# Optimization experiments

Measured on AMD Instinct MI355X. Metric: run time of the kernel, lower is better.

## Reference

```python
import jax, jax.numpy as jnp
import numpy as np

H = 8          # multihead_num (also groups of the Conv1d)
LN_EPS = 1e-5  # torch.nn.LayerNorm default


def _gconv(x, w):
    """Grouped Conv1d, kernel=3, stride=1, 'same' reflect padding, no bias.
    x: [B, C_in, L], w: [C_out, C_in//H, K] (torch OIH layout)."""
    xp = jnp.pad(x, ((0, 0), (0, 0), (1, 1)), mode='reflect')
    return jax.lax.conv_general_dilated(
        xp, w, window_strides=(1,), padding='VALID',
        feature_group_count=H, dimension_numbers=('NCH', 'OIH', 'NCH'))


def setup_inputs() -> dict:
    key = jax.random.key(0)
    ks = jax.random.split(key, 5)
    B, C, L = 8, 512, 1024
    q = jax.random.normal(ks[0], (B, C, L), jnp.float32)
    k = jax.random.normal(ks[1], (B, C, L), jnp.float32)
    # causal mask: 1 above the diagonal -> -1e9 subtracted pre-softmax
    mask = jnp.triu(jnp.ones((L, L), jnp.float32), k=1)
    # init_params: std = sqrt(2 / (C_out + C_in/groups))
    std = float(np.sqrt(2.0 / (C + C // H)))
    wq = jax.random.normal(ks[2], (C, C // H, 3), jnp.float32) * std
    wk = jax.random.normal(ks[3], (C, C // H, 3), jnp.float32) * std
    wv = jax.random.normal(ks[4], (C, C // H, 3), jnp.float32) * std
    gamma = jnp.ones((C,), jnp.float32)
    beta = jnp.zeros((C,), jnp.float32)
    return {"q": q, "k": k, "mask": mask, "wq": wq, "wk": wk, "wv": wv,
            "gamma": gamma, "beta": beta}


def reference(q, k, mask, wq, wk, wv, gamma, beta):
    init = q                               # residual branch, [B, C, L]
    B, C, L = q.shape
    D = C // H                             # head dim
    v = k                                  # inputs list of length 2 -> v = k

    qh = _gconv(q, wq).reshape(B, H, D, L)  # split(dim=1)+cat(dim=0) == head axis
    kh = _gconv(k, wk).reshape(B, H, D, L)
    vh = _gconv(v, wv).reshape(B, H, D, L)

    # scores: q^T k per head; NOTE: scaled by sqrt(multihead_num), as in source
    scores = jnp.einsum('bhdl,bhdm->bhlm', qh, kh) / jnp.sqrt(
        jnp.asarray(H, qh.dtype))
    scores = scores - 1e9 * mask           # mask broadcast over [B, H]
    att = jax.nn.softmax(scores, axis=-1)  # dropout p=0.0 -> identity

    # o = att @ v^T, then concat heads along channel (head-major order)
    o = jnp.einsum('bhlm,bhdm->blhd', att, vh).reshape(B, L, C)

    # residual add + LayerNorm over channel dim
    x = o + jnp.swapaxes(init, 1, 2)       # [B, L, C]
    mu = jnp.mean(x, axis=-1, keepdims=True)
    var = jnp.mean(jnp.square(x - mu), axis=-1, keepdims=True)
    y = (x - mu) * jax.lax.rsqrt(var + LN_EPS) * gamma + beta
    return jnp.swapaxes(y, 1, 2)           # [B, C, L]
```

## Files before the change

kernel.cpp:

```cpp
#include <hip/hip_runtime.h>
#include <math.h>

#define H 8
#define B 8
#define C 512
#define L 1024
#define D 64
#define LDK 72

typedef __attribute__((ext_vector_type(4))) float f32x4;
typedef __attribute__((ext_vector_type(8))) short bf16x8;

static __device__ __forceinline__ short f2bf(float x) {
    union { float f; unsigned u; } v; v.f = x;
    unsigned r = v.u + 0x7FFFu + ((v.u >> 16) & 1u);
    return (short)(r >> 16);
}
static __device__ __forceinline__ short f2bf_fast(float x) {
    union { float f; unsigned u; } v; v.f = x;
    return (short)((v.u + 0x8000u) >> 16);
}
static __device__ __forceinline__ int pack2(short a, short b) {
    return (int)((unsigned short)a | ((unsigned)(unsigned short)b << 16));
}
static __device__ __forceinline__ float bfs2f(short v) {
    union { unsigned u; float f; } w; w.u = ((unsigned)(unsigned short)v) << 16;
    return w.f;
}
static __device__ __forceinline__ void async16(const void* g, void* s) {
    __builtin_amdgcn_global_load_lds(
        (const __attribute__((address_space(1))) int*)g,
        (__attribute__((address_space(3))) int*)s, 16, 0, 0);
}

__global__ __launch_bounds__(256) void wprep_kernel(
    const float* __restrict__ wq, const float* __restrict__ wk,
    const float* __restrict__ wv, short* __restrict__ wtg)
{
    int idx = blockIdx.x * 256 + threadIdx.x;
    int jj    = idx & 7;
    int quad  = (idx >> 3) & 3;
    int d     = (idx >> 5) & 63;
    int r     = idx >> 11;
    int khalf = r & 1;  r >>= 1;
    int t     = r % 3;  r /= 3;
    int h     = r & 7;
    int conv  = r >> 3;
    const float* w = (conv == 0) ? wq : (conv == 1) ? wk : wv;
    int j_in = khalf * 32 + quad * 8 + jj;
    float v = w[(h * 64 + d) * 192 + j_in * 3 + t];
    if (conv == 0) v *= 0.51012254f;
    wtg[idx] = f2bf(v);
}

__global__ __launch_bounds__(256) void conv_kv_kernel(
    const float* __restrict__ k, const short* __restrict__ wtg,
    short* __restrict__ kh, short* __restrict__ vh)
{
    int bx   = blockIdx.x;
    int xcd  = bx & 7;
    int g    = bx >> 3;
    int bh   = xcd + 8 * (g & 7);
    int tile = g >> 3;
    int h    = bh & 7;
    int b    = bh >> 3;

    __shared__ __align__(16) short xT[66 * LDK];

    int l0  = tile * 64;
    int tid = threadIdx.x;
    int wave = tid >> 6, lane = tid & 63;
    int n = lane & 15, quad = lane >> 4;

    const float* xb = k + (size_t)(b * C + h * 64) * L + l0;

    const short* wb0 = wtg + (size_t)((1 * 8 + h) * 6) * 2048;
    const short* wb1 = wtg + (size_t)((2 * 8 + h) * 6) * 2048;
    bf16x8 wf[3][2], wf2[3][2];
    #pragma unroll
    for (int t = 0; t < 3; t++)
        #pragma unroll
        for (int kk = 0; kk < 2; kk++) {
            wf[t][kk]  = *(const bf16x8*)(wb0 + (t * 2 + kk) * 2048
                                          + (wave * 16 + n) * 32 + quad * 8);
            wf2[t][kk] = *(const bf16x8*)(wb1 + (t * 2 + kk) * 2048
                                          + (wave * 16 + n) * 32 + quad * 8);
        }

    {
        #pragma unroll
        for (int s = 0; s < 4; s++) {
            int idx = tid + s * 256;
            int j = idx >> 4, seg = idx & 15;
            float4 v = *(const float4*)(xb + j * L + seg * 4);
            int p = 1 + seg * 4;
            xT[(p + 0) * LDK + j] = f2bf(v.x);
            xT[(p + 1) * LDK + j] = f2bf(v.y);
            xT[(p + 2) * LDK + j] = f2bf(v.z);
            xT[(p + 3) * LDK + j] = f2bf(v.w);
        }
        if (tid < 64) {
            int gl = (l0 == 0) ? 1 : (l0 - 1);
            xT[0 * LDK + tid] = f2bf(k[(size_t)(b * C + h * 64 + tid) * L + gl]);
        } else if (tid < 128) {
            int j2 = tid - 64;
            int gl = (l0 + 64 >= L) ? (L - 2) : (l0 + 64);
            xT[65 * LDK + j2] = f2bf(k[(size_t)(b * C + h * 64 + j2) * L + gl]);
        }
    }
    __syncthreads();

    f32x4 acc[4], acc2[4];
    #pragma unroll
    for (int bl = 0; bl < 4; bl++) {
        acc[bl]  = (f32x4){0.f, 0.f, 0.f, 0.f};
        acc2[bl] = (f32x4){0.f, 0.f, 0.f, 0.f};
    }

    #pragma unroll
    for (int bl = 0; bl < 4; bl++)
        #pragma unroll
        for (int t = 0; t < 3; t++)
            #pragma unroll
            for (int kk = 0; kk < 2; kk++) {
                bf16x8 bf = *(const bf16x8*)&xT[(bl * 16 + n + t) * LDK
                                                + kk * 32 + quad * 8];
                acc[bl]  = __builtin_amdgcn_mfma_f32_16x16x32_bf16(
                    wf[t][kk],  bf, acc[bl],  0, 0, 0);
                acc2[bl] = __builtin_amdgcn_mfma_f32_16x16x32_bf16(
                    wf2[t][kk], bf, acc2[bl], 0, 0, 0);
            }

    {
        short* ob = kh + ((size_t)(bh * 16 + tile)) * 4096;
        int ch = wave * 2 + (quad >> 1);
        #pragma unroll
        for (int bl = 0; bl < 4; bl++) {
            int l = bl * 16 + n;
            int phys = ch ^ (l & 7);
            int2 v;
            v.x = pack2(f2bf(acc[bl][0]), f2bf(acc[bl][1]));
            v.y = pack2(f2bf(acc[bl][2]), f2bf(acc[bl][3]));
            *(int2*)&ob[l * 64 + phys * 8 + (quad & 1) * 4] = v;
        }
    }
    __syncthreads();
    #pragma unroll
    for (int bl = 0; bl < 4; bl++)
        #pragma unroll
        for (int r = 0; r < 4; r++) {
            int d = wave * 16 + quad * 4 + r;
            int l = bl * 16 + n;
            int phys = (bl * 2 + (n >> 3)) ^ (d & 7);
            xT[d * 64 + phys * 8 + (n & 7)] = f2bf(acc2[bl][r]);
        }
    __syncthreads();
    short* vb = vh + ((size_t)(bh * 16 + tile)) * 4096;
    #pragma unroll
    for (int jj = 0; jj < 2; jj++) {
        int i = tid + jj * 256;
        *(int4*)(vb + i * 8) = *(const int4*)&xT[i * 8];
    }
}

__global__ __launch_bounds__(256, 4) void flash_kernel(
    const float* __restrict__ q, const short* __restrict__ wtg,
    const short* __restrict__ kh, const short* __restrict__ vh,
    short* __restrict__ ot)
{
    __shared__ __align__(16) short lds[20480];
    short* xT = &lds[4096];

    int bx  = blockIdx.x;
    int xcd = bx & 7;
    int g   = bx >> 3;
    int bh  = xcd + 8 * (g & 7);
    int qt  = 15 - (g >> 3);
    int h  = bh & 7, b = bh >> 3;

    int tid  = threadIdx.x;
    int wave = tid >> 6, lane = tid & 63;
    int n    = lane & 15, quad = lane >> 4;
    int l0   = qt * 64;

    {
        const float* xb = q + (size_t)(b * C + h * 64) * L + l0;
        const short* wb0 = wtg + (size_t)((0 * 8 + h) * 6) * 2048;
        bf16x8 wf[3][2];
        #pragma unroll
        for (int t = 0; t < 3; t++)
            #pragma unroll
            for (int kk = 0; kk < 2; kk++)
                wf[t][kk] = *(const bf16x8*)(wb0 + (t * 2 + kk) * 2048
                                             + (wave * 16 + n) * 32 + quad * 8);
        #pragma unroll
        for (int s = 0; s < 4; s++) {
            int idx = tid + s * 256;
            int j = idx >> 4, seg = idx & 15;
            float4 v = *(const float4*)(xb + j * L + seg * 4);
            int p = 1 + seg * 4;
            xT[(p + 0) * LDK + j] = f2bf(v.x);
            xT[(p + 1) * LDK + j] = f2bf(v.y);
            xT[(p + 2) * LDK + j] = f2bf(v.z);
            xT[(p + 3) * LDK + j] = f2bf(v.w);
        }
        if (tid < 64) {
            int gl = (l0 == 0) ? 1 : (l0 - 1);
            xT[0 * LDK + tid] = f2bf(q[(size_t)(b * C + h * 64 + tid) * L + gl]);
        } else if (tid < 128) {
            int j2 = tid - 64;
            int gl = (l0 + 64 >= L) ? (L - 2) : (l0 + 64);
            xT[65 * LDK + j2] = f2bf(q[(size_t)(b * C + h * 64 + j2) * L + gl]);
        }
        __syncthreads();

        f32x4 acc[4];
        #pragma unroll
        for (int bl = 0; bl < 4; bl++) acc[bl] = (f32x4){0.f, 0.f, 0.f, 0.f};
        #pragma unroll
        for (int bl = 0; bl < 4; bl++)
            #pragma unroll
            for (int t = 0; t < 3; t++)
                #pragma unroll
                for (int kk = 0; kk < 2; kk++) {
                    bf16x8 bf = *(const bf16x8*)&xT[(bl * 16 + n + t) * LDK
                                                    + kk * 32 + quad * 8];
                    acc[bl] = __builtin_amdgcn_mfma_f32_16x16x32_bf16(
                        wf[t][kk], bf, acc[bl], 0, 0, 0);
                }
        __syncthreads();
        int ch = wave * 2 + (quad >> 1);
        #pragma unroll
        for (int bl = 0; bl < 4; bl++) {
            int l = bl * 16 + n;
            int phys = ch ^ (l & 7);
            int2 v;
            v.x = pack2(f2bf(acc[bl][0]), f2bf(acc[bl][1]));
            v.y = pack2(f2bf(acc[bl][2]), f2bf(acc[bl][3]));
            *(int2*)&lds[l * 64 + phys * 8 + (quad & 1) * 4] = v;
        }
    }

    const short* Kbase = kh + (size_t)bh * 65536;
    const short* Vbase = vh + (size_t)bh * 65536;

    {
        int ci = wave * 64 + lane;
        async16((const int4*)Kbase + ci,        lds + 4096 + wave * 512);
        async16((const int4*)Kbase + ci + 256,  lds + 4096 + 2048 + wave * 512);
        async16((const int4*)Vbase + ci,        lds + 8192 + wave * 512);
        async16((const int4*)Vbase + ci + 256,  lds + 8192 + 2048 + wave * 512);
    }
    __syncthreads();

    int ph0 = quad ^ (n & 7);
    int ph1 = (quad + 4) ^ (n & 7);

    bf16x8 qa0 = *(const bf16x8*)&lds[(wave * 16 + n) * 64 + ph0 * 8];
    bf16x8 qa1 = *(const bf16x8*)&lds[(wave * 16 + n) * 64 + ph1 * 8];

    const bf16x8 ones = {16256,16256,16256,16256,16256,16256,16256,16256};

    f32x4 O0 = {0.f,0.f,0.f,0.f}, O1 = O0, O2 = O0, O3 = O0;
    f32x4 Lacc = {0.f,0.f,0.f,0.f};

    int prow   = wave * 16 + n;
    int pswz   = n & 7;

    for (int kt = 0; kt <= qt; kt++) {
        if (kt > 0) __syncthreads();
        if (kt < qt) {
            const short* Kg = Kbase + (size_t)(kt + 1) * 4096;
            const short* Vg = Vbase + (size_t)(kt + 1) * 4096;
            int koff = 4096 + (((kt + 1) & 1)) * 8192;
            int ci = wave * 64 + lane;
            async16((const int4*)Kg + ci,       lds + koff + wave * 512);
            async16((const int4*)Kg + ci + 256, lds + koff + 2048 + wave * 512);
            async16((const int4*)Vg + ci,       lds + koff + 4096 + wave * 512);
            async16((const int4*)Vg + ci + 256, lds + koff + 4096 + 2048 + wave * 512);
        }
        const short* Kb = lds + 4096 + (kt & 1) * 8192;
        const short* Vb = Kb + 4096;

        f32x4 s[4];
        #pragma unroll
        for (int bk = 0; bk < 4; bk++) {
            int row = bk * 16 + n;
            bf16x8 kb0 = *(const bf16x8*)&Kb[row * 64 + ph0 * 8];
            bf16x8 kb1 = *(const bf16x8*)&Kb[row * 64 + ph1 * 8];
            f32x4 acc = {0.f,0.f,0.f,0.f};
            acc = __builtin_amdgcn_mfma_f32_16x16x32_bf16(kb0, qa0, acc, 0, 0, 0);
            acc = __builtin_amdgcn_mfma_f32_16x16x32_bf16(kb1, qa1, acc, 0, 0, 0);
            s[bk] = acc;
        }

        if (kt == qt) {
            #pragma unroll
            for (int bk = 0; bk < 4; bk++)
                #pragma unroll
                for (int r = 0; r < 4; r++)
                    if (bk * 16 + quad * 4 + r > wave * 16 + n)
                        s[bk][r] = -INFINITY;
        }

        #pragma unroll
        for (int bk = 0; bk < 4; bk++) {
            int pch = (bk * 2 + (quad >> 1)) ^ pswz;
            int2 v;
            v.x = pack2(f2bf_fast(__builtin_amdgcn_exp2f(s[bk][0] - 20.f)),
                        f2bf_fast(__builtin_amdgcn_exp2f(s[bk][1] - 20.f)));
            v.y = pack2(f2bf_fast(__builtin_amdgcn_exp2f(s[bk][2] - 20.f)),
                        f2bf_fast(__builtin_amdgcn_exp2f(s[bk][3] - 20.f)));
            *(int2*)&lds[prow * 64 + pch * 8 + (quad & 1) * 4] = v;
        }

        bf16x8 pa0 = *(const bf16x8*)&lds[prow * 64 + ph0 * 8];
        bf16x8 pa1 = *(const bf16x8*)&lds[prow * 64 + ph1 * 8];

        Lacc = __builtin_amdgcn_mfma_f32_16x16x32_bf16(pa0, ones, Lacc, 0, 0, 0);
        Lacc = __builtin_amdgcn_mfma_f32_16x16x32_bf16(pa1, ones, Lacc, 0, 0, 0);

        #pragma unroll
        for (int bk = 0; bk < 4; bk++) {
            int row = bk * 16 + n;
            bf16x8 v0 = *(const bf16x8*)&Vb[row * 64 + ph0 * 8];
            bf16x8 v1 = *(const bf16x8*)&Vb[row * 64 + ph1 * 8];
            f32x4* Op = (bk == 0) ? &O0 : (bk == 1) ? &O1 : (bk == 2) ? &O2 : &O3;
            *Op = __builtin_amdgcn_mfma_f32_16x16x32_bf16(pa0, v0, *Op, 0, 0, 0);
            *Op = __builtin_amdgcn_mfma_f32_16x16x32_bf16(pa1, v1, *Op, 0, 0, 0);
        }
    }

    float inv[4];
    #pragma unroll
    for (int r = 0; r < 4; r++) inv[r] = 1.f / Lacc[r];

    __syncthreads();
    short* Eb = lds + 4096;
    #pragma unroll
    for (int bk = 0; bk < 4; bk++) {
        f32x4* Op = (bk == 0) ? &O0 : (bk == 1) ? &O1 : (bk == 2) ? &O2 : &O3;
        #pragma unroll
        for (int r = 0; r < 4; r++)
            Eb[(bk * 16 + n) * LDK + wave * 16 + quad * 4 + r] =
                f2bf_fast((*Op)[r] * inv[r]);
    }
    __syncthreads();
    #pragma unroll
    for (int jj = 0; jj < 2; jj++) {
        int i = tid + jj * 256;
        int d = i >> 3, seg = i & 7;
        int4 v = *(const int4*)&Eb[d * LDK + seg * 8];
        *(int4*)(ot + ((size_t)(b * C) + h * 64 + d) * L + qt * 64 + seg * 8) = v;
    }
}

__global__ __launch_bounds__(512) void ln_kernel(
    const short* __restrict__ ot, const float* __restrict__ q,
    const float* __restrict__ gamma, const float* __restrict__ beta,
    float* __restrict__ y)
{
    int bx = blockIdx.x;
    int tile = bx & 31;
    int b = bx >> 5;
    int l0 = tile * 32;
    int tid = threadIdx.x;
    int li_ = tid & 31, cs = tid >> 5;

    __shared__ float sp[16][33], ssp[16][33];
    __shared__ float mu_s[32], rs_s[32];

    size_t base = ((size_t)b * C + cs * 32) * L + l0 + li_;
    const short* otp = ot + base;
    const float* qp  = q + base;

    float xr[32];
    float s = 0.f, ss = 0.f;
    #pragma unroll
    for (int cc = 0; cc < 32; cc++) {
        float x = bfs2f(otp[(size_t)cc * L]) + qp[(size_t)cc * L];
        xr[cc] = x;
        s += x; ss += x * x;
    }
    sp[cs][li_] = s; ssp[cs][li_] = ss;
    __syncthreads();
    if (tid < 32) {
        float t1 = 0.f, t2 = 0.f;
        #pragma unroll
        for (int j = 0; j < 16; j++) { t1 += sp[j][tid]; t2 += ssp[j][tid]; }
        float mean = t1 * (1.f / 512.f);
        float var  = t2 * (1.f / 512.f) - mean * mean;
        mu_s[tid] = mean;
        rs_s[tid] = rsqrtf(var + 1e-5f);
    }
    __syncthreads();
    float mu = mu_s[li_], rs = rs_s[li_];
    float* yp = y + base;
    #pragma unroll
    for (int cc = 0; cc < 32; cc++) {
        int c = cs * 32 + cc;
        yp[(size_t)cc * L] = (xr[cc] - mu) * rs * gamma[c] + beta[c];
    }
}

extern "C" void kernel_launch(void* const* d_in, const int* in_sizes, int n_in,
                              void* d_out, int out_size, void* d_ws, size_t ws_size,
                              hipStream_t stream)
{
    const float* q     = (const float*)d_in[0];
    const float* k     = (const float*)d_in[1];
    const float* wq    = (const float*)d_in[3];
    const float* wk    = (const float*)d_in[4];
    const float* wv    = (const float*)d_in[5];
    const float* gamma = (const float*)d_in[6];
    const float* beta  = (const float*)d_in[7];
    float* y = (float*)d_out;

    const size_t N = (size_t)B * H * L * D;
    short* kh  = (short*)d_ws;
    short* vh  = kh + N;
    short* ot  = vh + N;
    short* wtg = ot + N;

    wprep_kernel<<<1152, 256, 0, stream>>>(wq, wk, wv, wtg);
    conv_kv_kernel<<<B * H * (L / 64), 256, 0, stream>>>(k, wtg, kh, vh);
    flash_kernel<<<B * H * (L / 64), 256, 0, stream>>>(q, wtg, kh, vh, ot);
    ln_kernel<<<B * (L / 32), 512, 0, stream>>>(ot, q, gamma, beta, y);
}
```

Before: 127.9 us.

## Fuse weight prep into conv kernels and residual add into flash epilogue

Removes the separate weight-preparation kernel: each conv and flash block now loads its fp32 weight rows directly and converts them to bf16 fragments in registers. The flash epilogue stages the output in fp32 LDS, adds the residual q there, and writes the sum as bf16, so the LayerNorm kernel no longer reads q. This saves a launch and one fp32 read pass of q in the LN kernel. In exchange, weights are converted redundantly in every block, and the residual is now rounded to bf16 before LayerNorm, which lowers precision.

Result: slower. 135.3 us (+5.8%).

```diff
diff --git a/kernel.cpp b/kernel.cpp
--- a/kernel.cpp
+++ b/kernel.cpp
@@ -7,6 +7,7 @@
 #define L 1024
 #define D 64
 #define LDK 72
+#define LDKF 68
 
 typedef __attribute__((ext_vector_type(4))) float f32x4;
 typedef __attribute__((ext_vector_type(8))) short bf16x8;
@@ -33,28 +34,28 @@
         (__attribute__((address_space(3))) int*)s, 16, 0, 0);
 }
 
-__global__ __launch_bounds__(256) void wprep_kernel(
-    const float* __restrict__ wq, const float* __restrict__ wk,
-    const float* __restrict__ wv, short* __restrict__ wtg)
+static __device__ __forceinline__ void load_wfrag(
+    const float* __restrict__ wrow,
+    int quad, float scale, bf16x8 wf[3][2])
 {
-    int idx = blockIdx.x * 256 + threadIdx.x;
-    int jj    = idx & 7;
-    int quad  = (idx >> 3) & 3;
-    int d     = (idx >> 5) & 63;
-    int r     = idx >> 11;
-    int khalf = r & 1;  r >>= 1;
-    int t     = r % 3;  r /= 3;
-    int h     = r & 7;
-    int conv  = r >> 3;
-    const float* w = (conv == 0) ? wq : (conv == 1) ? wk : wv;
-    int j_in = khalf * 32 + quad * 8 + jj;
-    float v = w[(h * 64 + d) * 192 + j_in * 3 + t];
-    if (conv == 0) v *= 0.51012254f;
-    wtg[idx] = f2bf(v);
+    #pragma unroll
+    for (int kk = 0; kk < 2; kk++) {
+        float buf[24];
+        #pragma unroll
+        for (int m = 0; m < 6; m++)
+            *(float4*)&buf[m * 4] =
+                *(const float4*)(wrow + kk * 96 + quad * 24 + m * 4);
+        #pragma unroll
+        for (int t = 0; t < 3; t++)
+            #pragma unroll
+            for (int jj = 0; jj < 8; jj++)
+                wf[t][kk][jj] = f2bf(buf[jj * 3 + t] * scale);
+    }
 }
 
 __global__ __launch_bounds__(256) void conv_kv_kernel(
-    const float* __restrict__ k, const short* __restrict__ wtg,
+    const float* __restrict__ k,
+    const float* __restrict__ wk, const float* __restrict__ wv,
     short* __restrict__ kh, short* __restrict__ vh)
 {
     int bx   = blockIdx.x;
@@ -74,18 +75,9 @@
 
     const float* xb = k + (size_t)(b * C + h * 64) * L + l0;
 
-    const short* wb0 = wtg + (size_t)((1 * 8 + h) * 6) * 2048;
-    const short* wb1 = wtg + (size_t)((2 * 8 + h) * 6) * 2048;
     bf16x8 wf[3][2], wf2[3][2];
-    #pragma unroll
-    for (int t = 0; t < 3; t++)
-        #pragma unroll
-        for (int kk = 0; kk < 2; kk++) {
-            wf[t][kk]  = *(const bf16x8*)(wb0 + (t * 2 + kk) * 2048
-                                          + (wave * 16 + n) * 32 + quad * 8);
-            wf2[t][kk] = *(const bf16x8*)(wb1 + (t * 2 + kk) * 2048
-                                          + (wave * 16 + n) * 32 + quad * 8);
-        }
+    load_wfrag(wk + (size_t)(h * 64 + wave * 16 + n) * 192, quad, 1.0f, wf);
+    load_wfrag(wv + (size_t)(h * 64 + wave * 16 + n) * 192, quad, 1.0f, wf2);
 
     {
         #pragma unroll
@@ -164,7 +156,7 @@
 }
 
 __global__ __launch_bounds__(256, 4) void flash_kernel(
-    const float* __restrict__ q, const short* __restrict__ wtg,
+    const float* __restrict__ q, const float* __restrict__ wq,
     const short* __restrict__ kh, const short* __restrict__ vh,
     short* __restrict__ ot)
 {
@@ -185,14 +177,9 @@
 
     {
         const float* xb = q + (size_t)(b * C + h * 64) * L + l0;
-        const short* wb0 = wtg + (size_t)((0 * 8 + h) * 6) * 2048;
         bf16x8 wf[3][2];
-        #pragma unroll
-        for (int t = 0; t < 3; t++)
-            #pragma unroll
-            for (int kk = 0; kk < 2; kk++)
-                wf[t][kk] = *(const bf16x8*)(wb0 + (t * 2 + kk) * 2048
-                                             + (wave * 16 + n) * 32 + quad * 8);
+        load_wfrag(wq + (size_t)(h * 64 + wave * 16 + n) * 192, quad,
+                   0.51012254f, wf);
         #pragma unroll
         for (int s = 0; s < 4; s++) {
             int idx = tid + s * 256;
@@ -336,27 +323,37 @@
     for (int r = 0; r < 4; r++) inv[r] = 1.f / Lacc[r];
 
     __syncthreads();
-    short* Eb = lds + 4096;
+    float* Ebf = (float*)(lds + 4096);
     #pragma unroll
     for (int bk = 0; bk < 4; bk++) {
         f32x4* Op = (bk == 0) ? &O0 : (bk == 1) ? &O1 : (bk == 2) ? &O2 : &O3;
         #pragma unroll
         for (int r = 0; r < 4; r++)
-            Eb[(bk * 16 + n) * LDK + wave * 16 + quad * 4 + r] =
-                f2bf_fast((*Op)[r] * inv[r]);
+            Ebf[(bk * 16 + n) * LDKF + wave * 16 + quad * 4 + r] =
+                (*Op)[r] * inv[r];
     }
     __syncthreads();
     #pragma unroll
     for (int jj = 0; jj < 2; jj++) {
         int i = tid + jj * 256;
         int d = i >> 3, seg = i & 7;
-        int4 v = *(const int4*)&Eb[d * LDK + seg * 8];
+        const float* Ef = &Ebf[d * LDKF + seg * 8];
+        const float* qp = q + ((size_t)(b * C) + h * 64 + d) * L + qt * 64 + seg * 8;
+        float4 o0 = *(const float4*)Ef;
+        float4 o1 = *(const float4*)(Ef + 4);
+        float4 q0 = *(const float4*)qp;
+        float4 q1 = *(const float4*)(qp + 4);
+        int4 v;
+        v.x = pack2(f2bf(o0.x + q0.x), f2bf(o0.y + q0.y));
+        v.y = pack2(f2bf(o0.z + q0.z), f2bf(o0.w + q0.w));
+        v.z = pack2(f2bf(o1.x + q1.x), f2bf(o1.y + q1.y));
+        v.w = pack2(f2bf(o1.z + q1.z), f2bf(o1.w + q1.w));
         *(int4*)(ot + ((size_t)(b * C) + h * 64 + d) * L + qt * 64 + seg * 8) = v;
     }
 }
 
 __global__ __launch_bounds__(512) void ln_kernel(
-    const short* __restrict__ ot, const float* __restrict__ q,
+    const short* __restrict__ ot,
     const float* __restrict__ gamma, const float* __restrict__ beta,
     float* __restrict__ y)
 {
@@ -372,13 +369,12 @@
 
     size_t base = ((size_t)b * C + cs * 32) * L + l0 + li_;
     const short* otp = ot + base;
-    const float* qp  = q + base;
 
     float xr[32];
     float s = 0.f, ss = 0.f;
     #pragma unroll
     for (int cc = 0; cc < 32; cc++) {
-        float x = bfs2f(otp[(size_t)cc * L]) + qp[(size_t)cc * L];
+        float x = bfs2f(otp[(size_t)cc * L]);
         xr[cc] = x;
         s += x; ss += x * x;
     }
@@ -420,10 +416,8 @@
     short* kh  = (short*)d_ws;
     short* vh  = kh + N;
     short* ot  = vh + N;
-    short* wtg = ot + N;
-
-    wprep_kernel<<<1152, 256, 0, stream>>>(wq, wk, wv, wtg);
-    conv_kv_kernel<<<B * H * (L / 64), 256, 0, stream>>>(k, wtg, kh, vh);
-    flash_kernel<<<B * H * (L / 64), 256, 0, stream>>>(q, wtg, kh, vh, ot);
-    ln_kernel<<<B * (L / 32), 512, 0, stream>>>(ot, q, gamma, beta, y);
-}
+
+    conv_kv_kernel<<<B * H * (L / 64), 256, 0, stream>>>(k, wk, wv, kh, vh);
+    flash_kernel<<<B * H * (L / 64), 256, 0, stream>>>(q, wq, kh, vh, ot);
+    ln_kernel<<<B * (L / 32), 512, 0, stream>>>(ot, gamma, beta, y);
+}
```
